# Performance work log

Hardware: AMD Instinct MI355X
Metric: run time of the kernel (lower is better)

The kernel has to match this reference:

```python
import jax, jax.numpy as jnp
import numpy as np

N_NODES = 50000
N_EDGES = 800000
D_IN = 128
D_HID = 128
D_OUT = 128
N_LAYERS = 2
NEG_SLOPE = 0.2


def leaky(x):
    return jnp.where(x >= 0, x, NEG_SLOPE * x)


def setup_inputs() -> dict:
    key = jax.random.key(0)
    ks = jax.random.split(key, 12)
    s = 1.0 / np.sqrt(D_HID)
    feats = jax.random.normal(ks[0], (N_NODES, D_IN), dtype=jnp.float32)
    src = jax.random.randint(ks[1], (N_EDGES,), 0, N_NODES)
    dst = jax.random.randint(ks[2], (N_EDGES,), 0, N_NODES)
    # SIRConv params per layer: W_Q (dst), W_K (src), W_R (output proj)
    Wq = jax.random.normal(ks[3], (N_LAYERS, D_IN, D_HID), dtype=jnp.float32) * s
    bq = jnp.zeros((N_LAYERS, D_HID), dtype=jnp.float32)
    Wk = jax.random.normal(ks[4], (N_LAYERS, D_IN, D_HID), dtype=jnp.float32) * s
    bk = jnp.zeros((N_LAYERS, D_HID), dtype=jnp.float32)
    Wr = jax.random.normal(ks[5], (N_LAYERS, D_HID, D_HID), dtype=jnp.float32) * s
    br = jnp.zeros((N_LAYERS, D_HID), dtype=jnp.float32)
    # Jumping-knowledge readouts: one per entry of feats_list (input + each layer);
    # input_dim == hidden_dim so weights stack along the leading axis.
    Wro = jax.random.normal(ks[6], (N_LAYERS + 1, D_HID, D_OUT), dtype=jnp.float32) * s
    bro = jnp.zeros((N_LAYERS + 1, D_OUT), dtype=jnp.float32)
    return {"feats": feats, "Wq": Wq, "bq": bq, "Wk": Wk, "bk": bk,
            "Wr": Wr, "br": br, "Wro": Wro, "bro": bro,
            "src": src, "dst": dst}


def reference(feats, Wq, bq, Wk, bk, Wr, br, Wro, bro, src, dst):
    # mean-aggregation denominator: in-degree, clamped to 1
    deg = jax.ops.segment_sum(jnp.ones((N_EDGES,), jnp.float32), dst,
                              num_segments=N_NODES)
    denom = jnp.maximum(deg, 1.0)[:, None]  # [N, 1]

    feats_list = [feats]
    h = feats
    for i in range(N_LAYERS):
        hq = h @ Wq[i] + bq[i]          # [N, H] (dst transform)
        hk = h @ Wk[i] + bk[i]          # [N, H] (src transform)
        m = leaky(hq[dst] + hk[src])    # [E, H] contextualized messages
        agg = jax.ops.segment_sum(m, dst, num_segments=N_NODES) / denom
        h = agg @ Wr[i] + br[i]         # conv output (+ residual = 0)
        h = leaky(h)                    # norm='none', dropout=0
        feats_list.append(h)

    # jumping-knowledge readout: sum of per-stage linear readouts
    score = feats_list[0] @ Wro[0] + bro[0]
    for i in range(1, N_LAYERS + 1):
        score = score + feats_list[i] @ Wro[i] + bro[i]
    return score
```

## Files before the change

kernel.cpp:

```cpp
#include <hip/hip_runtime.h>

#define NN 50000
#define NE 800000
#define D 128
#define NEG 0.2f

#define NBLK1 256
#define TILE1 3125
#define NB2 196
#define CAP2 8192
#define NT64 782

#define SB_PREP 576
#define SB_CONV 6250
#define SB_HIST NBLK1
#define SB_TOTAL (SB_PREP + SB_CONV + SB_HIST)

typedef short bf8_t __attribute__((ext_vector_type(8)));
typedef float f4_t __attribute__((ext_vector_type(4)));

__device__ __forceinline__ unsigned short f2bf(float f) {
  unsigned int u = __float_as_uint(f);
  return (unsigned short)((u + 0x7FFF + ((u >> 16) & 1)) >> 16);
}
__device__ __forceinline__ float bf2f(unsigned int b) { return __uint_as_float(b << 16); }

__device__ __forceinline__ f4_t MF(bf8_t a, bf8_t b, f4_t c) {
  return __builtin_amdgcn_mfma_f32_16x16x32_bf16(a, b, c, 0, 0, 0);
}


__device__ __forceinline__ void stage_w(unsigned short* wbuf,
                                        const unsigned short* __restrict__ WT, int t) {
#pragma unroll
  for (int i = 0; i < 8; ++i) {
    int idx8 = t + i * 256;
    *(uint4*)(wbuf + idx8 * 8) = *(const uint4*)(WT + idx8 * 8);
  }
}

__device__ __forceinline__ void load_a16(const unsigned short* __restrict__ A,
                                         int base, int l15, int quad, bf8_t (&afr)[4]) {
  int r = base + l15;
  if (r >= NN) r = NN - 1;
  const unsigned short* p = A + (size_t)r * D + quad * 8;
#pragma unroll
  for (int kc = 0; kc < 4; ++kc) afr[kc] = *(const bf8_t*)(p + kc * 32);
}

__device__ __forceinline__ void tile16(const unsigned short* wbuf, const bf8_t (&afr)[4],
                                       int l15, int quad, f4_t (&acc)[8]) {
#pragma unroll
  for (int kc = 0; kc < 4; ++kc)
#pragma unroll
    for (int nt = 0; nt < 8; ++nt) {
      bf8_t b = *(const bf8_t*)(wbuf + (nt * 16 + l15) * D + kc * 32 + quad * 8);
      acc[nt] = MF(afr[kc], b, acc[nt]);
    }
}

__global__ __launch_bounds__(256) void setup(
    const float* __restrict__ Wq, const float* __restrict__ Wk,
    const float* __restrict__ Wr, const float* __restrict__ Wro,
    const float* __restrict__ feats, const int* __restrict__ dst,
    unsigned short* __restrict__ WT, unsigned short* __restrict__ x0,
    int* __restrict__ H) {
  __shared__ int cnt[NB2];
  const int b = blockIdx.x;
  const int t = threadIdx.x;
  if (b < SB_PREP) {
    const int m = b >> 6, xb = b & 63;
    const float* src;
    if (m < 2) src = Wq + m * D * D;
    else if (m < 4) src = Wk + (m - 2) * D * D;
    else if (m < 6) src = Wr + (m - 4) * D * D;
    else src = Wro + (m - 6) * D * D;
    const int n = xb * 2 + (t >> 7);
    const int k = t & 127;
    WT[(size_t)m * D * D + n * D + k] = f2bf(src[k * D + n]);
  } else if (b < SB_PREP + SB_CONV) {
    int i = ((b - SB_PREP) * 256 + t) * 4;
    float4 v = *(const float4*)(feats + i);
    ushort4 o = {f2bf(v.x), f2bf(v.y), f2bf(v.z), f2bf(v.w)};
    *(ushort4*)(x0 + i) = o;
  } else {
    const int blk = b - SB_PREP - SB_CONV;
    if (t < NB2) cnt[t] = 0;
    __syncthreads();
    const int beg = blk * TILE1, end = beg + TILE1;
    for (int i = beg + t; i < end; i += 256) atomicAdd(&cnt[dst[i] >> 8], 1);
    __syncthreads();
    if (t < NB2) H[t * NBLK1 + blk] = cnt[t];
  }
}

__global__ __launch_bounds__(256) void p1_scan(const int* __restrict__ H,
                                               int* __restrict__ gofs) {
  __shared__ int sd[256];
  __shared__ int wsum[4];
  const int bin = blockIdx.x;
  const int t = threadIdx.x;
  const int wave = t >> 6, lane = t & 63;
  int part = 0;
  for (int b2 = 0; b2 < bin; ++b2) part += H[b2 * NBLK1 + t];
  for (int off = 32; off; off >>= 1) part += __shfl_down(part, off, 64);
  if (lane == 0) wsum[wave] = part;
  __syncthreads();
  const int base = wsum[0] + wsum[1] + wsum[2] + wsum[3];
  int x = H[bin * NBLK1 + t];
  sd[t] = x;
  __syncthreads();
  int acc = x;
  for (int off = 1; off < 256; off <<= 1) {
    int y = (t >= off) ? sd[t - off] : 0;
    __syncthreads();
    acc += y;
    sd[t] = acc;
    __syncthreads();
  }
  gofs[bin * NBLK1 + t] = base + (acc - x);
}

__global__ __launch_bounds__(256) void p1_scatter(const int* __restrict__ src,
                                                  const int* __restrict__ dst,
                                                  const int* __restrict__ gofs,
                                                  unsigned int* __restrict__ ebuf) {
  __shared__ int lofs[NB2];
  const int t = threadIdx.x;
  const int blk = blockIdx.x;
  if (t < NB2) lofs[t] = gofs[t * NBLK1 + blk];
  __syncthreads();
  const int beg = blk * TILE1, end = beg + TILE1;
  for (int i = beg + t; i < end; i += 256) {
    unsigned int d = (unsigned int)dst[i];
    int pos = atomicAdd(&lofs[d >> 8], 1);
    ebuf[pos] = (unsigned int)src[i] | (d << 16);
  }
}

__global__ __launch_bounds__(256) void sort_qk0(
    const int* __restrict__ gofs, const unsigned int* __restrict__ ebuf,
    int* __restrict__ ssrc, int* __restrict__ rowptr, int* __restrict__ deg,
    const unsigned short* __restrict__ x0,
    const unsigned short* __restrict__ WTq, const float* __restrict__ bq_,
    const unsigned short* __restrict__ WTk, const float* __restrict__ bk_,
    unsigned short* __restrict__ hq, unsigned short* __restrict__ hk) {
  __shared__ __align__(16) unsigned char smraw[35840];
  const int t = threadIdx.x;
  const int gx = blockIdx.x;
  if (gx < NB2) {
    int* cnt = (int*)smraw;
    int* fill = cnt + 256;
    int* sd = fill + 256;
    unsigned int* sorted = (unsigned int*)(sd + 256);
    const int b = gx;
    const int beg = gofs[b * NBLK1];
    const int end = (b + 1 < NB2) ? gofs[(b + 1) * NBLK1] : NE;
    const int n = end - beg;
    cnt[t] = 0;
    __syncthreads();
    for (int i = beg + t; i < end; i += 256)
      atomicAdd(&cnt[(ebuf[i] >> 16) & 255], 1);
    __syncthreads();
    int x = cnt[t];
    sd[t] = x;
    __syncthreads();
    int acc = x;
    for (int off = 1; off < 256; off <<= 1) {
      int y = (t >= off) ? sd[t - off] : 0;
      __syncthreads();
      acc += y;
      sd[t] = acc;
      __syncthreads();
    }
    const int excl = acc - x;
    fill[t] = excl;
    __syncthreads();
    for (int i = beg + t; i < end; i += 256) {
      unsigned int p = ebuf[i];
      int pos = atomicAdd(&fill[(p >> 16) & 255], 1);
      if (pos < CAP2) sorted[pos] = p;
    }
    __syncthreads();
    for (int i = t; i < n; i += 256) ssrc[beg + i] = (int)(sorted[i] & 0xFFFFu);
    const int node = (b << 8) + t;
    if (node < NN) {
      rowptr[node] = beg + excl;
      deg[node] = x;
    }
    if (b == 0 && t == 0) rowptr[NN] = NE;
  } else {
    unsigned short* wbuf = (unsigned short*)smraw;
    const int g = gx - NB2;
    const int sel = g & 1, tile = g >> 1;
    const int wave = t >> 6, lane = t & 63;
    const int l15 = lane & 15, quad = lane >> 4;
    const int base = tile * 64 + wave * 16;
    stage_w(wbuf, sel ? WTk : WTq, t);
    bf8_t afr[4];
    load_a16(x0, base, l15, quad, afr);
    __syncthreads();
    f4_t acc[8] = {};
    tile16(wbuf, afr, l15, quad, acc);
    const float* bias = sel ? bk_ : bq_;
    unsigned short* C = sel ? hk : hq;
#pragma unroll
    for (int nt = 0; nt < 8; ++nt) {
      int col = nt * 16 + l15;
      float bb = bias[col];
#pragma unroll
      for (int reg = 0; reg < 4; ++reg) {
        int row = base + quad * 4 + reg;
        if (row < NN) C[(size_t)row * D + col] = f2bf(acc[nt][reg] + bb);
      }
    }
  }
}

#define PROC(kb)                                                     \
  {                                                                  \
    float m;                                                         \
    m = q[0] + bf2f(kb.x & 0xFFFFu); a[0] += m >= 0.f ? m : NEG * m; \
    m = q[1] + bf2f(kb.x >> 16);     a[1] += m >= 0.f ? m : NEG * m; \
    m = q[2] + bf2f(kb.y & 0xFFFFu); a[2] += m >= 0.f ? m : NEG * m; \
    m = q[3] + bf2f(kb.y >> 16);     a[3] += m >= 0.f ? m : NEG * m; \
    m = q[4] + bf2f(kb.z & 0xFFFFu); a[4] += m >= 0.f ? m : NEG * m; \
    m = q[5] + bf2f(kb.z >> 16);     a[5] += m >= 0.f ? m : NEG * m; \
    m = q[6] + bf2f(kb.w & 0xFFFFu); a[6] += m >= 0.f ? m : NEG * m; \
    m = q[7] + bf2f(kb.w >> 16);     a[7] += m >= 0.f ? m : NEG * m; \
  }

__global__ __launch_bounds__(256) void aggregate(
    const int* __restrict__ rowptr, const int* __restrict__ ssrc,
    const int* __restrict__ deg,
    const unsigned short* __restrict__ hq, const unsigned short* __restrict__ hk,
    unsigned short* __restrict__ ag) {
  const int wave = threadIdx.x >> 6, lane = threadIdx.x & 63;
  const int v = blockIdx.x * 4 + wave;
  if (v >= NN) return;
  const int sub = lane & 15, grp = lane >> 4;
  const int beg = rowptr[v], end = rowptr[v + 1];

  uint4 qb = *(const uint4*)(hq + (size_t)v * D + sub * 8);
  float q[8];
  q[0] = bf2f(qb.x & 0xFFFFu); q[1] = bf2f(qb.x >> 16);
  q[2] = bf2f(qb.y & 0xFFFFu); q[3] = bf2f(qb.y >> 16);
  q[4] = bf2f(qb.z & 0xFFFFu); q[5] = bf2f(qb.z >> 16);
  q[6] = bf2f(qb.w & 0xFFFFu); q[7] = bf2f(qb.w >> 16);

  float a[8] = {0.f, 0.f, 0.f, 0.f, 0.f, 0.f, 0.f, 0.f};
  int e = beg + grp;
  for (; e + 4 < end; e += 8) {
    int s0 = ssrc[e];
    int s1 = ssrc[e + 4];
    uint4 k0 = *(const uint4*)(hk + (size_t)s0 * D + sub * 8);
    uint4 k1 = *(const uint4*)(hk + (size_t)s1 * D + sub * 8);
    PROC(k0);
    PROC(k1);
  }
  if (e < end) {
    int s0 = ssrc[e];
    uint4 k0 = *(const uint4*)(hk + (size_t)s0 * D + sub * 8);
    PROC(k0);
  }
#pragma unroll
  for (int j = 0; j < 8; ++j) {
    a[j] += __shfl_xor(a[j], 16, 64);
    a[j] += __shfl_xor(a[j], 32, 64);
  }
  if (grp == 0) {
    float inv = 1.f / fmaxf((float)deg[v], 1.f);
    uint4 o;
    o.x = (unsigned int)f2bf(a[0] * inv) | ((unsigned int)f2bf(a[1] * inv) << 16);
    o.y = (unsigned int)f2bf(a[2] * inv) | ((unsigned int)f2bf(a[3] * inv) << 16);
    o.z = (unsigned int)f2bf(a[4] * inv) | ((unsigned int)f2bf(a[5] * inv) << 16);
    o.w = (unsigned int)f2bf(a[6] * inv) | ((unsigned int)f2bf(a[7] * inv) << 16);
    *(uint4*)(ag + (size_t)v * D + sub * 8) = o;
  }
}

template <bool LEAKY>
__global__ __launch_bounds__(256) void gemm64(const unsigned short* __restrict__ A,
                                              const unsigned short* __restrict__ WT0,
                                              const float* __restrict__ b0,
                                              unsigned short* __restrict__ C0,
                                              const unsigned short* __restrict__ WT1,
                                              const float* __restrict__ b1,
                                              unsigned short* __restrict__ C1) {
  __shared__ unsigned short wbuf[D * D];
  const int t = threadIdx.x, wave = t >> 6, lane = t & 63;
  const int l15 = lane & 15, quad = lane >> 4;
  const int sel = blockIdx.x;
  const unsigned short* WT = sel ? WT1 : WT0;
  const float* bias = sel ? b1 : b0;
  unsigned short* C = sel ? C1 : C0;
  const int base = blockIdx.y * 64 + wave * 16;

  stage_w(wbuf, WT, t);
  bf8_t afr[4];
  load_a16(A, base, l15, quad, afr);
  __syncthreads();

  f4_t acc[8] = {};
  tile16(wbuf, afr, l15, quad, acc);

#pragma unroll
  for (int nt = 0; nt < 8; ++nt) {
    int col = nt * 16 + l15;
    float b = bias[col];
#pragma unroll
    for (int reg = 0; reg < 4; ++reg) {
      int row = base + quad * 4 + reg;
      if (row < NN) {
        float v = acc[nt][reg] + b;
        if (LEAKY) v = v >= 0.f ? v : NEG * v;
        C[(size_t)row * D + col] = f2bf(v);
      }
    }
  }
}

__global__ __launch_bounds__(256) void readout(const unsigned short* __restrict__ x0,
                                               const unsigned short* __restrict__ h1,
                                               const unsigned short* __restrict__ h2,
                                               const unsigned short* __restrict__ WTro,
                                               const float* __restrict__ bro_,
                                               float* __restrict__ out) {
  __shared__ unsigned short wbuf[D * D];
  const int t = threadIdx.x, wave = t >> 6, lane = t & 63;
  const int l15 = lane & 15, quad = lane >> 4;
  const int base = blockIdx.x * 64 + wave * 16;
  const unsigned short* As[3] = {x0, h1, h2};

  f4_t acc[8] = {};
#pragma unroll
  for (int ph = 0; ph < 3; ++ph) {
    stage_w(wbuf, WTro + (size_t)ph * D * D, t);
    bf8_t afr[4];
    load_a16(As[ph], base, l15, quad, afr);
    __syncthreads();
    tile16(wbuf, afr, l15, quad, acc);
    if (ph < 2) __syncthreads();
  }

#pragma unroll
  for (int nt = 0; nt < 8; ++nt) {
    int col = nt * 16 + l15;
    float b = bro_[col] + bro_[D + col] + bro_[2 * D + col];
#pragma unroll
    for (int reg = 0; reg < 4; ++reg) {
      int row = base + quad * 4 + reg;
      if (row < NN) out[(size_t)row * D + col] = acc[nt][reg] + b;
    }
  }
}

extern "C" void kernel_launch(void* const* d_in, const int* in_sizes, int n_in,
                              void* d_out, int out_size, void* d_ws, size_t ws_size,
                              hipStream_t stream) {
  const float* feats = (const float*)d_in[0];
  const float* Wq = (const float*)d_in[1];
  const float* bq = (const float*)d_in[2];
  const float* Wk = (const float*)d_in[3];
  const float* bk = (const float*)d_in[4];
  const float* Wr = (const float*)d_in[5];
  const float* br = (const float*)d_in[6];
  const float* Wro = (const float*)d_in[7];
  const float* bro = (const float*)d_in[8];
  const int* src = (const int*)d_in[9];
  const int* dst = (const int*)d_in[10];
  float* out = (float*)d_out;

  size_t off = 0;
  char* base = (char*)d_ws;
  auto alloc = [&](size_t bytes) -> void* {
    void* p = base + off;
    off += (bytes + 255) & ~(size_t)255;
    return p;
  };
  int* H = (int*)alloc((size_t)NB2 * NBLK1 * 4);
  int* gofs = (int*)alloc((size_t)NB2 * NBLK1 * 4);
  unsigned int* ebuf = (unsigned int*)alloc((size_t)NE * 4);
  int* ssrc = (int*)alloc((size_t)NE * 4);
  int* rowptr = (int*)alloc((size_t)(NN + 1) * 4);
  int* deg = (int*)alloc((size_t)NN * 4);
  unsigned short* WT = (unsigned short*)alloc((size_t)9 * D * D * 2);
  unsigned short* x0 = (unsigned short*)alloc((size_t)NN * D * 2);
  unsigned short* hq = (unsigned short*)alloc((size_t)NN * D * 2);
  unsigned short* hk = (unsigned short*)alloc((size_t)NN * D * 2);
  unsigned short* ag = (unsigned short*)alloc((size_t)NN * D * 2);
  unsigned short* h1 = (unsigned short*)alloc((size_t)NN * D * 2);
  unsigned short* h2 = (unsigned short*)alloc((size_t)NN * D * 2);

  const size_t WM = (size_t)D * D;
  const int ab = (NN + 3) / 4;

  setup<<<SB_TOTAL, 256, 0, stream>>>(Wq, Wk, Wr, Wro, feats, dst, WT, x0, H);
  p1_scan<<<NB2, 256, 0, stream>>>(H, gofs);
  p1_scatter<<<NBLK1, 256, 0, stream>>>(src, dst, gofs, ebuf);
  sort_qk0<<<NB2 + 2 * NT64, 256, 0, stream>>>(gofs, ebuf, ssrc, rowptr, deg,
                                               x0, WT + 0 * WM, bq, WT + 2 * WM, bk,
                                               hq, hk);
  aggregate<<<ab, 256, 0, stream>>>(rowptr, ssrc, deg, hq, hk, ag);
  gemm64<true><<<dim3(1, NT64), 256, 0, stream>>>(ag, WT + 4 * WM, br, h1,
                                                  WT + 4 * WM, br, h1);
  gemm64<false><<<dim3(2, NT64), 256, 0, stream>>>(h1, WT + 1 * WM, bq + D, hq,
                                                   WT + 3 * WM, bk + D, hk);
  aggregate<<<ab, 256, 0, stream>>>(rowptr, ssrc, deg, hq, hk, ag);
  gemm64<true><<<dim3(1, NT64), 256, 0, stream>>>(ag, WT + 5 * WM, br + D, h2,
                                                  WT + 5 * WM, br + D, h2);
  readout<<<NT64, 256, 0, stream>>>(x0, h1, h2, WT + 6 * WM, bro, out);
}
```

Measured before the change: 317.4 us.

## Store hk in FP8 and fuse GEMMs and readout into aggregation kernels

Key features hk are now stored as FP8, which halves the bytes fetched by the random gathers in aggregation. The Wr GEMM is fused with the next layer's Q/K GEMMs, and the final Wr GEMM with its readout, by staging the intermediate tile in swizzled shared memory. The per-stage readout GEMMs now run as extra blocks inside the aggregation launches and accumulate into the output. Together this removes several launches and intermediate round-trips through global memory, at the cost of FP8 precision loss on hk and read-modify-write traffic on the fp32 output.

```diff
diff --git a/kernel.cpp b/kernel.cpp
--- a/kernel.cpp
+++ b/kernel.cpp
@@ -10,20 +10,30 @@
 #define NB2 196
 #define CAP2 8192
 #define NT64 782
+#define ABLK 12500
 
 #define SB_PREP 576
 #define SB_CONV 6250
-#define SB_HIST NBLK1
-#define SB_TOTAL (SB_PREP + SB_CONV + SB_HIST)
+#define SB_TOTAL (SB_PREP + SB_CONV + NBLK1)
 
 typedef short bf8_t __attribute__((ext_vector_type(8)));
 typedef float f4_t __attribute__((ext_vector_type(4)));
+typedef float f2_t __attribute__((ext_vector_type(2)));
 
 __device__ __forceinline__ unsigned short f2bf(float f) {
   unsigned int u = __float_as_uint(f);
   return (unsigned short)((u + 0x7FFF + ((u >> 16) & 1)) >> 16);
 }
 __device__ __forceinline__ float bf2f(unsigned int b) { return __uint_as_float(b << 16); }
+
+__device__ __forceinline__ unsigned char f2fp8(float v) {
+  int p = __builtin_amdgcn_cvt_pk_fp8_f32(v, v, 0, false);
+  return (unsigned char)(p & 0xFF);
+}
+template <bool HI>
+__device__ __forceinline__ f2_t fp8pair(unsigned int w) {
+  return __builtin_amdgcn_cvt_pk_f32_fp8((int)w, HI);
+}
 
 __device__ __forceinline__ f4_t MF(bf8_t a, bf8_t b, f4_t c) {
   return __builtin_amdgcn_mfma_f32_16x16x32_bf16(a, b, c, 0, 0, 0);
@@ -48,6 +58,16 @@
   for (int kc = 0; kc < 4; ++kc) afr[kc] = *(const bf8_t*)(p + kc * 32);
 }
 
+__device__ __forceinline__ void load_a16_swz(const unsigned short* hbuf,
+                                             int wave, int l15, int quad, bf8_t (&afr)[4]) {
+  int r = wave * 16 + l15;
+#pragma unroll
+  for (int kc = 0; kc < 4; ++kc) {
+    int chunk = kc * 4 + quad;
+    afr[kc] = *(const bf8_t*)(hbuf + r * D + ((chunk ^ (r & 7)) << 3));
+  }
+}
+
 __device__ __forceinline__ void tile16(const unsigned short* wbuf, const bf8_t (&afr)[4],
                                        int l15, int quad, f4_t (&acc)[8]) {
 #pragma unroll
@@ -57,6 +77,40 @@
       bf8_t b = *(const bf8_t*)(wbuf + (nt * 16 + l15) * D + kc * 32 + quad * 8);
       acc[nt] = MF(afr[kc], b, acc[nt]);
     }
+}
+
+__device__ __forceinline__ void epi_bf(const f4_t (&acc)[8], const float* __restrict__ bias,
+                                       unsigned short* __restrict__ C, int base,
+                                       int l15, int quad, bool leaky) {
+#pragma unroll
+  for (int nt = 0; nt < 8; ++nt) {
+    int col = nt * 16 + l15;
+    float b = bias[col];
+#pragma unroll
+    for (int reg = 0; reg < 4; ++reg) {
+      int row = base + quad * 4 + reg;
+      if (row < NN) {
+        float v = acc[nt][reg] + b;
+        if (leaky) v = v >= 0.f ? v : NEG * v;
+        C[(size_t)row * D + col] = f2bf(v);
+      }
+    }
+  }
+}
+
+__device__ __forceinline__ void epi_fp8(const f4_t (&acc)[8], const float* __restrict__ bias,
+                                        unsigned char* __restrict__ C, int base,
+                                        int l15, int quad) {
+#pragma unroll
+  for (int nt = 0; nt < 8; ++nt) {
+    int col = nt * 16 + l15;
+    float b = bias[col];
+#pragma unroll
+    for (int reg = 0; reg < 4; ++reg) {
+      int row = base + quad * 4 + reg;
+      if (row < NN) C[(size_t)row * D + col] = f2fp8(acc[nt][reg] + b);
+    }
+  }
 }
 
 __global__ __launch_bounds__(256) void setup(
@@ -144,7 +198,7 @@
     const unsigned short* __restrict__ x0,
     const unsigned short* __restrict__ WTq, const float* __restrict__ bq_,
     const unsigned short* __restrict__ WTk, const float* __restrict__ bk_,
-    unsigned short* __restrict__ hq, unsigned short* __restrict__ hk) {
+    unsigned short* __restrict__ hq, unsigned char* __restrict__ hk8) {
   __shared__ __align__(16) unsigned char smraw[35840];
   const int t = threadIdx.x;
   const int gx = blockIdx.x;
@@ -202,155 +256,209 @@
     __syncthreads();
     f4_t acc[8] = {};
     tile16(wbuf, afr, l15, quad, acc);
-    const float* bias = sel ? bk_ : bq_;
-    unsigned short* C = sel ? hk : hq;
+    if (sel) epi_fp8(acc, bk_, hk8, base, l15, quad);
+    else epi_bf(acc, bq_, hq, base, l15, quad, false);
+  }
+}
+
+#define PROC8(kb)                                                  \
+  {                                                                \
+    f2_t p; float m;                                               \
+    p = fp8pair<false>(kb.x);                                      \
+    m = q[0] + p.x; a[0] += m >= 0.f ? m : NEG * m;                \
+    m = q[1] + p.y; a[1] += m >= 0.f ? m : NEG * m;                \
+    p = fp8pair<true>(kb.x);                                       \
+    m = q[2] + p.x; a[2] += m >= 0.f ? m : NEG * m;                \
+    m = q[3] + p.y; a[3] += m >= 0.f ? m : NEG * m;                \
+    p = fp8pair<false>(kb.y);                                      \
+    m = q[4] + p.x; a[4] += m >= 0.f ? m : NEG * m;                \
+    m = q[5] + p.y; a[5] += m >= 0.f ? m : NEG * m;                \
+    p = fp8pair<true>(kb.y);                                       \
+    m = q[6] + p.x; a[6] += m >= 0.f ? m : NEG * m;                \
+    m = q[7] + p.y; a[7] += m >= 0.f ? m : NEG * m;                \
+  }
+
+template <bool ACCUM>
+__global__ __launch_bounds__(256) void agg_ro(
+    const int* __restrict__ rowptr, const int* __restrict__ ssrc,
+    const int* __restrict__ deg,
+    const unsigned short* __restrict__ hq, const unsigned char* __restrict__ hk8,
+    unsigned short* __restrict__ ag,
+    const unsigned short* __restrict__ Aro, const unsigned short* __restrict__ WTro,
+    const float* __restrict__ bro_, float* __restrict__ out) {
+  __shared__ unsigned short wbuf[D * D];
+  const int t = threadIdx.x;
+  const int gx = blockIdx.x;
+  if (gx < ABLK) {
+    const int wave = t >> 6, lane = t & 63;
+    const int v = gx * 4 + wave;
+    const int sub = lane & 15, grp = lane >> 4;
+    const int beg = rowptr[v], end = rowptr[v + 1];
+
+    uint4 qb = *(const uint4*)(hq + (size_t)v * D + sub * 8);
+    float q[8];
+    q[0] = bf2f(qb.x & 0xFFFFu); q[1] = bf2f(qb.x >> 16);
+    q[2] = bf2f(qb.y & 0xFFFFu); q[3] = bf2f(qb.y >> 16);
+    q[4] = bf2f(qb.z & 0xFFFFu); q[5] = bf2f(qb.z >> 16);
+    q[6] = bf2f(qb.w & 0xFFFFu); q[7] = bf2f(qb.w >> 16);
+
+    float a[8] = {0.f, 0.f, 0.f, 0.f, 0.f, 0.f, 0.f, 0.f};
+    int e = beg + grp;
+    for (; e + 4 < end; e += 8) {
+      int s0 = ssrc[e];
+      int s1 = ssrc[e + 4];
+      uint2 k0 = *(const uint2*)(hk8 + (size_t)s0 * D + sub * 8);
+      uint2 k1 = *(const uint2*)(hk8 + (size_t)s1 * D + sub * 8);
+      PROC8(k0);
+      PROC8(k1);
+    }
+    if (e < end) {
+      int s0 = ssrc[e];
+      uint2 k0 = *(const uint2*)(hk8 + (size_t)s0 * D + sub * 8);
+      PROC8(k0);
+    }
+#pragma unroll
+    for (int j = 0; j < 8; ++j) {
+      a[j] += __shfl_xor(a[j], 16, 64);
+      a[j] += __shfl_xor(a[j], 32, 64);
+    }
+    if (grp == 0) {
+      float inv = 1.f / fmaxf((float)deg[v], 1.f);
+      uint4 o;
+      o.x = (unsigned int)f2bf(a[0] * inv) | ((unsigned int)f2bf(a[1] * inv) << 16);
+      o.y = (unsigned int)f2bf(a[2] * inv) | ((unsigned int)f2bf(a[3] * inv) << 16);
+      o.z = (unsigned int)f2bf(a[4] * inv) | ((unsigned int)f2bf(a[5] * inv) << 16);
+      o.w = (unsigned int)f2bf(a[6] * inv) | ((unsigned int)f2bf(a[7] * inv) << 16);
+      *(uint4*)(ag + (size_t)v * D + sub * 8) = o;
+    }
+  } else {
+    const int wave = t >> 6, lane = t & 63;
+    const int l15 = lane & 15, quad = lane >> 4;
+    const int base = (gx - ABLK) * 64 + wave * 16;
+    stage_w(wbuf, WTro, t);
+    bf8_t afr[4];
+    load_a16(Aro, base, l15, quad, afr);
+    __syncthreads();
+    f4_t acc[8] = {};
+    tile16(wbuf, afr, l15, quad, acc);
 #pragma unroll
     for (int nt = 0; nt < 8; ++nt) {
       int col = nt * 16 + l15;
-      float bb = bias[col];
+      float b = bro_[col];
 #pragma unroll
       for (int reg = 0; reg < 4; ++reg) {
         int row = base + quad * 4 + reg;
-        if (row < NN) C[(size_t)row * D + col] = f2bf(acc[nt][reg] + bb);
+        if (row < NN) {
+          float v = acc[nt][reg] + b;
+          float* p = out + (size_t)row * D + col;
+          if (ACCUM) v += *p;
+          *p = v;
+        }
       }
     }
   }
 }
 
-#define PROC(kb)                                                     \
-  {                                                                  \
-    float m;                                                         \
-    m = q[0] + bf2f(kb.x & 0xFFFFu); a[0] += m >= 0.f ? m : NEG * m; \
-    m = q[1] + bf2f(kb.x >> 16);     a[1] += m >= 0.f ? m : NEG * m; \
-    m = q[2] + bf2f(kb.y & 0xFFFFu); a[2] += m >= 0.f ? m : NEG * m; \
-    m = q[3] + bf2f(kb.y >> 16);     a[3] += m >= 0.f ? m : NEG * m; \
-    m = q[4] + bf2f(kb.z & 0xFFFFu); a[4] += m >= 0.f ? m : NEG * m; \
-    m = q[5] + bf2f(kb.z >> 16);     a[5] += m >= 0.f ? m : NEG * m; \
-    m = q[6] + bf2f(kb.w & 0xFFFFu); a[6] += m >= 0.f ? m : NEG * m; \
-    m = q[7] + bf2f(kb.w >> 16);     a[7] += m >= 0.f ? m : NEG * m; \
-  }
-
-__global__ __launch_bounds__(256) void aggregate(
-    const int* __restrict__ rowptr, const int* __restrict__ ssrc,
-    const int* __restrict__ deg,
-    const unsigned short* __restrict__ hq, const unsigned short* __restrict__ hk,
-    unsigned short* __restrict__ ag) {
-  const int wave = threadIdx.x >> 6, lane = threadIdx.x & 63;
-  const int v = blockIdx.x * 4 + wave;
-  if (v >= NN) return;
-  const int sub = lane & 15, grp = lane >> 4;
-  const int beg = rowptr[v], end = rowptr[v + 1];
-
-  uint4 qb = *(const uint4*)(hq + (size_t)v * D + sub * 8);
-  float q[8];
-  q[0] = bf2f(qb.x & 0xFFFFu); q[1] = bf2f(qb.x >> 16);
-  q[2] = bf2f(qb.y & 0xFFFFu); q[3] = bf2f(qb.y >> 16);
-  q[4] = bf2f(qb.z & 0xFFFFu); q[5] = bf2f(qb.z >> 16);
-  q[6] = bf2f(qb.w & 0xFFFFu); q[7] = bf2f(qb.w >> 16);
-
-  float a[8] = {0.f, 0.f, 0.f, 0.f, 0.f, 0.f, 0.f, 0.f};
-  int e = beg + grp;
-  for (; e + 4 < end; e += 8) {
-    int s0 = ssrc[e];
-    int s1 = ssrc[e + 4];
-    uint4 k0 = *(const uint4*)(hk + (size_t)s0 * D + sub * 8);
-    uint4 k1 = *(const uint4*)(hk + (size_t)s1 * D + sub * 8);
-    PROC(k0);
-    PROC(k1);
-  }
-  if (e < end) {
-    int s0 = ssrc[e];
-    uint4 k0 = *(const uint4*)(hk + (size_t)s0 * D + sub * 8);
-    PROC(k0);
-  }
-#pragma unroll
-  for (int j = 0; j < 8; ++j) {
-    a[j] += __shfl_xor(a[j], 16, 64);
-    a[j] += __shfl_xor(a[j], 32, 64);
-  }
-  if (grp == 0) {
-    float inv = 1.f / fmaxf((float)deg[v], 1.f);
-    uint4 o;
-    o.x = (unsigned int)f2bf(a[0] * inv) | ((unsigned int)f2bf(a[1] * inv) << 16);
-    o.y = (unsigned int)f2bf(a[2] * inv) | ((unsigned int)f2bf(a[3] * inv) << 16);
-    o.z = (unsigned int)f2bf(a[4] * inv) | ((unsigned int)f2bf(a[5] * inv) << 16);
-    o.w = (unsigned int)f2bf(a[6] * inv) | ((unsigned int)f2bf(a[7] * inv) << 16);
-    *(uint4*)(ag + (size_t)v * D + sub * 8) = o;
-  }
-}
-
-template <bool LEAKY>
-__global__ __launch_bounds__(256) void gemm64(const unsigned short* __restrict__ A,
-                                              const unsigned short* __restrict__ WT0,
-                                              const float* __restrict__ b0,
-                                              unsigned short* __restrict__ C0,
-                                              const unsigned short* __restrict__ WT1,
-                                              const float* __restrict__ b1,
-                                              unsigned short* __restrict__ C1) {
+__global__ __launch_bounds__(256) void r0qk1(
+    const unsigned short* __restrict__ ag,
+    const unsigned short* __restrict__ WTr, const float* __restrict__ br_,
+    const unsigned short* __restrict__ WTq, const float* __restrict__ bq_,
+    const unsigned short* __restrict__ WTk, const float* __restrict__ bk_,
+    unsigned short* __restrict__ h1, unsigned short* __restrict__ hq,
+    unsigned char* __restrict__ hk8) {
   __shared__ unsigned short wbuf[D * D];
+  __shared__ unsigned short hbuf[64 * D];
   const int t = threadIdx.x, wave = t >> 6, lane = t & 63;
   const int l15 = lane & 15, quad = lane >> 4;
-  const int sel = blockIdx.x;
-  const unsigned short* WT = sel ? WT1 : WT0;
-  const float* bias = sel ? b1 : b0;
-  unsigned short* C = sel ? C1 : C0;
-  const int base = blockIdx.y * 64 + wave * 16;
-
-  stage_w(wbuf, WT, t);
+  const int base = blockIdx.x * 64 + wave * 16;
+
+  stage_w(wbuf, WTr, t);
   bf8_t afr[4];
-  load_a16(A, base, l15, quad, afr);
-  __syncthreads();
-
+  load_a16(ag, base, l15, quad, afr);
+  __syncthreads();
   f4_t acc[8] = {};
   tile16(wbuf, afr, l15, quad, acc);
 
 #pragma unroll
   for (int nt = 0; nt < 8; ++nt) {
     int col = nt * 16 + l15;
-    float b = bias[col];
+    float b = br_[col];
+#pragma unroll
+    for (int reg = 0; reg < 4; ++reg) {
+      int rl = wave * 16 + quad * 4 + reg;
+      float v = acc[nt][reg] + b;
+      v = v >= 0.f ? v : NEG * v;
+      unsigned short s = f2bf(v);
+      hbuf[rl * D + (((col >> 3) ^ (rl & 7)) << 3) + (col & 7)] = s;
+      int row = blockIdx.x * 64 + rl;
+      if (row < NN) h1[(size_t)row * D + col] = s;
+    }
+  }
+  __syncthreads();
+  stage_w(wbuf, WTq, t);
+  __syncthreads();
+
+  load_a16_swz(hbuf, wave, l15, quad, afr);
+  f4_t acc2[8] = {};
+  tile16(wbuf, afr, l15, quad, acc2);
+  epi_bf(acc2, bq_, hq, base, l15, quad, false);
+  __syncthreads();
+  stage_w(wbuf, WTk, t);
+  __syncthreads();
+
+  f4_t acc3[8] = {};
+  tile16(wbuf, afr, l15, quad, acc3);
+  epi_fp8(acc3, bk_, hk8, base, l15, quad);
+}
+
+__global__ __launch_bounds__(256) void r1ro2(
+    const unsigned short* __restrict__ ag,
+    const unsigned short* __restrict__ WTr, const float* __restrict__ br_,
+    const unsigned short* __restrict__ WTro, const float* __restrict__ bro_,
+    float* __restrict__ out) {
+  __shared__ unsigned short wbuf[D * D];
+  __shared__ unsigned short hbuf[64 * D];
+  const int t = threadIdx.x, wave = t >> 6, lane = t & 63;
+  const int l15 = lane & 15, quad = lane >> 4;
+  const int base = blockIdx.x * 64 + wave * 16;
+
+  stage_w(wbuf, WTr, t);
+  bf8_t afr[4];
+  load_a16(ag, base, l15, quad, afr);
+  __syncthreads();
+  f4_t acc[8] = {};
+  tile16(wbuf, afr, l15, quad, acc);
+
+#pragma unroll
+  for (int nt = 0; nt < 8; ++nt) {
+    int col = nt * 16 + l15;
+    float b = br_[col];
+#pragma unroll
+    for (int reg = 0; reg < 4; ++reg) {
+      int rl = wave * 16 + quad * 4 + reg;
+      float v = acc[nt][reg] + b;
+      v = v >= 0.f ? v : NEG * v;
+      hbuf[rl * D + (((col >> 3) ^ (rl & 7)) << 3) + (col & 7)] = f2bf(v);
+    }
+  }
+  __syncthreads();
+  stage_w(wbuf, WTro, t);
+  __syncthreads();
+
+  load_a16_swz(hbuf, wave, l15, quad, afr);
+  f4_t acc2[8] = {};
+  tile16(wbuf, afr, l15, quad, acc2);
+#pragma unroll
+  for (int nt = 0; nt < 8; ++nt) {
+    int col = nt * 16 + l15;
+    float b = bro_[col];
 #pragma unroll
     for (int reg = 0; reg < 4; ++reg) {
       int row = base + quad * 4 + reg;
       if (row < NN) {
-        float v = acc[nt][reg] + b;
-        if (LEAKY) v = v >= 0.f ? v : NEG * v;
-        C[(size_t)row * D + col] = f2bf(v);
+        float* p = out + (size_t)row * D + col;
+        *p = *p + acc2[nt][reg] + b;
       }
-    }
-  }
-}
-
-__global__ __launch_bounds__(256) void readout(const unsigned short* __restrict__ x0,
-                                               const unsigned short* __restrict__ h1,
-                                               const unsigned short* __restrict__ h2,
-                                               const unsigned short* __restrict__ WTro,
-                                               const float* __restrict__ bro_,
-                                               float* __restrict__ out) {
-  __shared__ unsigned short wbuf[D * D];
-  const int t = threadIdx.x, wave = t >> 6, lane = t & 63;
-  const int l15 = lane & 15, quad = lane >> 4;
-  const int base = blockIdx.x * 64 + wave * 16;
-  const unsigned short* As[3] = {x0, h1, h2};
-
-  f4_t acc[8] = {};
-#pragma unroll
-  for (int ph = 0; ph < 3; ++ph) {
-    stage_w(wbuf, WTro + (size_t)ph * D * D, t);
-    bf8_t afr[4];
-    load_a16(As[ph], base, l15, quad, afr);
-    __syncthreads();
-    tile16(wbuf, afr, l15, quad, acc);
-    if (ph < 2) __syncthreads();
-  }
-
-#pragma unroll
-  for (int nt = 0; nt < 8; ++nt) {
-    int col = nt * 16 + l15;
-    float b = bro_[col] + bro_[D + col] + bro_[2 * D + col];
-#pragma unroll
-    for (int reg = 0; reg < 4; ++reg) {
-      int row = base + quad * 4 + reg;
-      if (row < NN) out[(size_t)row * D + col] = acc[nt][reg] + b;
     }
   }
 }
@@ -387,27 +495,25 @@
   unsigned short* WT = (unsigned short*)alloc((size_t)9 * D * D * 2);
   unsigned short* x0 = (unsigned short*)alloc((size_t)NN * D * 2);
   unsigned short* hq = (unsigned short*)alloc((size_t)NN * D * 2);
-  unsigned short* hk = (unsigned short*)alloc((size_t)NN * D * 2);
+  unsigned char* hk8 = (unsigned char*)alloc((size_t)NN * D);
   unsigned short* ag = (unsigned short*)alloc((size_t)NN * D * 2);
   unsigned short* h1 = (unsigned short*)alloc((size_t)NN * D * 2);
-  unsigned short* h2 = (unsigned short*)alloc((size_t)NN * D * 2);
 
   const size_t WM = (size_t)D * D;
-  const int ab = (NN + 3) / 4;
 
   setup<<<SB_TOTAL, 256, 0, stream>>>(Wq, Wk, Wr, Wro, feats, dst, WT, x0, H);
   p1_scan<<<NB2, 256, 0, stream>>>(H, gofs);
   p1_scatter<<<NBLK1, 256, 0, stream>>>(src, dst, gofs, ebuf);
   sort_qk0<<<NB2 + 2 * NT64, 256, 0, stream>>>(gofs, ebuf, ssrc, rowptr, deg,
                                                x0, WT + 0 * WM, bq, WT + 2 * WM, bk,
-                                               hq, hk);
-  aggregate<<<ab, 256, 0, stream>>>(rowptr, ssrc, deg, hq, hk, ag);
-  gemm64<true><<<dim3(1, NT64), 256, 0, stream>>>(ag, WT + 4 * WM, br, h1,
-                                                  WT + 4 * WM, br, h1);
-  gemm64<false><<<dim3(2, NT64), 256, 0, stream>>>(h1, WT + 1 * WM, bq + D, hq,
-                                                   WT + 3 * WM, bk + D, hk);
-  aggregate<<<ab, 256, 0, stream>>>(rowptr, ssrc, deg, hq, hk, ag);
-  gemm64<true><<<dim3(1, NT64), 256, 0, stream>>>(ag, WT + 5 * WM, br + D, h2,
-                                                  WT + 5 * WM, br + D, h2);
-  readout<<<NT64, 256, 0, stream>>>(x0, h1, h2, WT + 6 * WM, bro, out);
-}
+                                               hq, hk8);
+  agg_ro<false><<<ABLK + NT64, 256, 0, stream>>>(rowptr, ssrc, deg, hq, hk8, ag,
+                                                 x0, WT + 6 * WM, bro, out);
+  r0qk1<<<NT64, 256, 0, stream>>>(ag, WT + 4 * WM, br,
+                                  WT + 1 * WM, bq + D, WT + 3 * WM, bk + D,
+                                  h1, hq, hk8);
+  agg_ro<true><<<ABLK + NT64, 256, 0, stream>>>(rowptr, ssrc, deg, hq, hk8, ag,
+                                                h1, WT + 7 * WM, bro + D, out);
+  r1ro2<<<NT64, 256, 0, stream>>>(ag, WT + 5 * WM, br + D,
+                                  WT + 8 * WM, bro + 2 * D, out);
+}
```

Measured after the change: 364.7 us. 14.9% more time.
